# Optimization experiments

Hardware: AMD Instinct MI355X
Metric: run time of the kernel (lower is better)

The kernel has to match this reference:

```python
import jax, jax.numpy as jnp
import numpy as np
from jax import lax

VOCAB = 1000
TMAX = 1001  # max_episode_length + 1
L = 2048
H_GRU = 256


def setup_inputs() -> dict:
    key = jax.random.key(0)
    ks = jax.random.split(key, 40)
    g = lambda i, shape, s: jax.random.normal(ks[i], shape, dtype=jnp.float32) * s
    inp = {
        "x": jax.random.normal(ks[0], (1, 3, 124, 124), dtype=jnp.float32),
        "curr_instr": jax.random.randint(ks[1], (1, L), 0, VOCAB),
        "prev_instr": jax.random.randint(ks[2], (1, L), 0, VOCAB),
        "next_instr": jax.random.randint(ks[3], (1, L), 0, VOCAB),
        "tx": jax.random.randint(ks[4], (1,), 0, TMAX),
        "hx": jnp.zeros((1, 768), jnp.float32),
        "cx": jnp.zeros((1, 768), jnp.float32),
        # conv stack
        "conv1_w": g(5, (128, 3, 8, 8), 0.05), "conv1_b": jnp.zeros((128,), jnp.float32),
        "conv2_w": g(6, (64, 128, 4, 4), 0.03), "conv2_b": jnp.zeros((64,), jnp.float32),
        "conv3_w": g(7, (64, 64, 4, 4), 0.03), "conv3_b": jnp.zeros((64,), jnp.float32),
        # embeddings
        "emb": g(8, (VOCAB, 32), 0.1),
        "time_emb": g(9, (TMAX, 32), 0.1),
        # GRU (torch nn.GRU layout: 3*H rows for r,z,n)
        "gru_w_ih": g(10, (3 * H_GRU, 32), 0.1), "gru_w_hh": g(11, (3 * H_GRU, H_GRU), 0.06),
        "gru_b_ih": jnp.zeros((3 * H_GRU,), jnp.float32), "gru_b_hh": jnp.zeros((3 * H_GRU,), jnp.float32),
        # attention linear 256 -> 64
        "attn_w": g(12, (64, H_GRU), 0.06), "attn_b": jnp.zeros((64,), jnp.float32),
        # image-fusion linear 64*6*6 -> 256
        "lin_w": g(13, (256, 64 * 6 * 6), 0.02), "lin_b": jnp.zeros((256,), jnp.float32),
        # LSTMCell 768 -> 768 (torch layout: 4*H rows for i,f,g,o)
        "lstm_w_ih": g(14, (4 * 768, 768), 0.03), "lstm_w_hh": g(15, (4 * 768, 768), 0.03),
        "lstm_b_ih": jnp.zeros((4 * 768,), jnp.float32), "lstm_b_hh": jnp.zeros((4 * 768,), jnp.float32),
        # heads over [hx, time_emb] = 768 + 32 = 800
        "critic_w": g(16, (1, 800), 0.03), "critic_b": jnp.zeros((1,), jnp.float32),
        "actor_w": g(17, (4, 800), 0.01), "actor_b": jnp.zeros((4,), jnp.float32),
    }
    return inp


def _conv(x, w, b, s):
    return lax.conv_general_dilated(x, w, (s, s), "VALID") + b[None, :, None, None]


def reference(x, curr_instr, prev_instr, next_instr, tx, hx, cx,
              conv1_w, conv1_b, conv2_w, conv2_b, conv3_w, conv3_b,
              emb, time_emb, gru_w_ih, gru_w_hh, gru_b_ih, gru_b_hh,
              attn_w, attn_b, lin_w, lin_b,
              lstm_w_ih, lstm_w_hh, lstm_b_ih, lstm_b_hh,
              critic_w, critic_b, actor_w, actor_b):
    # image tower: [1,3,124,124] -> [1,64,6,6]
    h1 = jax.nn.relu(_conv(x, conv1_w, conv1_b, 4))
    h2 = jax.nn.relu(_conv(h1, conv2_w, conv2_b, 2))
    x_image_rep = jax.nn.relu(_conv(h2, conv3_w, conv3_b, 2))

    # three instruction sequences, encoded by a shared GRU (vmapped scan)
    tokens = jnp.stack([curr_instr[0], prev_instr[0], next_instr[0]])  # [3, L]

    def gru_encode(tok):
        xs = emb[tok]                               # [L, 32]
        gi_all = xs @ gru_w_ih.T + gru_b_ih         # precompute input gates [L, 3H]
        def step(h, gi):
            gh = h @ gru_w_hh.T + gru_b_hh
            i_r, i_z, i_n = jnp.split(gi, 3)
            h_r, h_z, h_n = jnp.split(gh, 3)
            r = jax.nn.sigmoid(i_r + h_r)
            z = jax.nn.sigmoid(i_z + h_z)
            n = jnp.tanh(i_n + r * h_n)
            return (1.0 - z) * n + z * h, None
        h, _ = lax.scan(step, jnp.zeros((H_GRU,), xs.dtype), gi_all)
        return h

    h3 = jax.vmap(gru_encode)(tokens)               # [3, 256]
    attn = jax.nn.sigmoid(h3 @ attn_w.T + attn_b)   # [3, 64]

    # BUG-FAITHFUL: original forward uses cached_computation['curr_x_attention']
    # for all three branches, so the three fused features are identical.
    curr_attn = attn[0][None, :, None, None]        # [1,64,1,1]
    fused = (x_image_rep * curr_attn).reshape(1, -1)  # [1, 2304]
    feat = jax.nn.relu(fused @ lin_w.T + lin_b)     # [1, 256]
    xcat = jnp.concatenate([feat, feat, feat], axis=1)  # [1, 768]

    # LSTMCell
    gates = xcat @ lstm_w_ih.T + lstm_b_ih + hx @ lstm_w_hh.T + lstm_b_hh  # [1, 3072]
    gi, gf, gg, go = jnp.split(gates, 4, axis=1)
    cx_new = jax.nn.sigmoid(gf) * cx + jax.nn.sigmoid(gi) * jnp.tanh(gg)
    hx_new = jax.nn.sigmoid(go) * jnp.tanh(cx_new)

    t = time_emb[tx].reshape(-1, 32)                # [1, 32]
    z = jnp.concatenate([hx_new, t], axis=1)        # [1, 800]
    critic = z @ critic_w.T + critic_b              # [1, 1]
    actor = z @ actor_w.T + actor_b                 # [1, 4]
    return critic, actor, hx_new, cx_new
```

## Files before the change

kernel.cpp:

```cpp
#include <hip/hip_runtime.h>
#include <hip/hip_bf16.h>
#include <stdint.h>


typedef _Float16 half8 __attribute__((ext_vector_type(8)));
typedef _Float16 half2v __attribute__((ext_vector_type(2)));
typedef float f32x4 __attribute__((ext_vector_type(4)));

__device__ __forceinline__ float sigm(float x) { return 1.0f / (1.0f + __expf(-x)); }
__device__ __forceinline__ float tanh_f(float x) { return 2.0f / (1.0f + __expf(-2.0f * x)) - 1.0f; }

__global__ void k_pack(const float* __restrict__ whh, uint32_t* __restrict__ wf16p) {
    int i = blockIdx.x * 256 + threadIdx.x;
    if (i >= 98304) return;
    half2v p = {(_Float16)whh[2 * i], (_Float16)whh[2 * i + 1]};
    wf16p[i] = __builtin_bit_cast(uint32_t, p);
}

__global__ void k_conv1(const float* __restrict__ x, const float* __restrict__ w,
                        const float* __restrict__ b, float* __restrict__ h1) {
    int idx = blockIdx.x * 256 + threadIdx.x;
    if (idx >= 128 * 30 * 30) return;
    int ox = idx % 30, oy = (idx / 30) % 30, oc = idx / 900;
    const float* wr = w + oc * 192;
    float acc = b[oc];
    for (int c = 0; c < 3; ++c)
        for (int ky = 0; ky < 8; ++ky) {
            const float* xr = x + (c * 124 + oy * 4 + ky) * 124 + ox * 4;
            const float* wk = wr + (c * 8 + ky) * 8;
#pragma unroll
            for (int kx = 0; kx < 8; ++kx) acc = fmaf(xr[kx], wk[kx], acc);
        }
    h1[idx] = fmaxf(acc, 0.0f);
}

__global__ void k_conv2(const float* __restrict__ h1, const float* __restrict__ w,
                        const float* __restrict__ b, float* __restrict__ h2) {
    int idx = blockIdx.x * 256 + threadIdx.x;
    if (idx >= 64 * 14 * 14) return;
    int ox = idx % 14, oy = (idx / 14) % 14, oc = idx / 196;
    float acc = b[oc];
    const float* wr = w + oc * 128 * 16;
    for (int c = 0; c < 128; ++c) {
#pragma unroll
        for (int ky = 0; ky < 4; ++ky) {
            const float* hr = h1 + (c * 30 + oy * 2 + ky) * 30 + ox * 2;
            const float* wk = wr + (c * 4 + ky) * 4;
#pragma unroll
            for (int kx = 0; kx < 4; ++kx) acc = fmaf(hr[kx], wk[kx], acc);
        }
    }
    h2[idx] = fmaxf(acc, 0.0f);
}

__global__ void k_conv3(const float* __restrict__ h2, const float* __restrict__ w,
                        const float* __restrict__ b, float* __restrict__ x3) {
    int idx = blockIdx.x * 256 + threadIdx.x;
    if (idx >= 64 * 6 * 6) return;
    int ox = idx % 6, oy = (idx / 6) % 6, oc = idx / 36;
    float acc = b[oc];
    const float* wr = w + oc * 64 * 16;
    for (int c = 0; c < 64; ++c) {
#pragma unroll
        for (int ky = 0; ky < 4; ++ky) {
            const float* hr = h2 + (c * 14 + oy * 2 + ky) * 14 + ox * 2;
            const float* wk = wr + (c * 4 + ky) * 4;
#pragma unroll
            for (int kx = 0; kx < 4; ++kx) acc = fmaf(hr[kx], wk[kx], acc);
        }
    }
    x3[idx] = fmaxf(acc, 0.0f);
}

__global__ void k_gi(const int* __restrict__ curr, const float* __restrict__ emb,
                     const float* __restrict__ wih, const float* __restrict__ bih,
                     float* __restrict__ gi) {
    int idx = blockIdx.x * 256 + threadIdx.x;
    int j = idx % 768, t = idx / 768;
    int tok = curr[t];
    const float4* e = (const float4*)(emb + tok * 32);
    const float4* wr = (const float4*)(wih + j * 32);
    float acc = bih[j];
#pragma unroll
    for (int k = 0; k < 8; ++k) {
        float4 ev = e[k], wv = wr[k];
        acc = fmaf(ev.x, wv.x, acc);
        acc = fmaf(ev.y, wv.y, acc);
        acc = fmaf(ev.z, wv.z, acc);
        acc = fmaf(ev.w, wv.w, acc);
    }
    gi[idx] = acc;
}

#define FOR8(X, nt) X(nt, 0) X(nt, 1) X(nt, 2) X(nt, 3) X(nt, 4) X(nt, 5) X(nt, 6) X(nt, 7)
#define FOR6(Y) Y(0) Y(1) Y(2) Y(3) Y(4) Y(5)

#define DECLB(nt, kt) uint4 b##nt##_##kt;
#define DECLBROW(nt) FOR8(DECLB, nt)
#define LOADB(nt, kt) b##nt##_##kt = wp4[nt * 512 + kt * 4 + quad];
#define LOADBROW(nt) FOR8(LOADB, nt)
#define TIEB(nt, kt) \
    asm volatile("" : "+v"(b##nt##_##kt.x), "+v"(b##nt##_##kt.y), "+v"(b##nt##_##kt.z), "+v"(b##nt##_##kt.w));
#define TIEBROW(nt) FOR8(TIEB, nt)
#define DECLBIAS(nt) const float bias##nt = bhh[wbase + nt * 16 + n16];
#define DECLACC(nt) f32x4 acc##nt;
#define ZEROACC(nt) acc##nt = (f32x4)(0.0f);
#define MF(nt, kt) \
    acc##nt = __builtin_amdgcn_mfma_f32_16x16x32_f16(a##kt, __builtin_bit_cast(half8, b##nt##_##kt), acc##nt, 0, 0, 0);
#define MFK(kt) MF(0, kt) MF(1, kt) MF(2, kt) MF(3, kt) MF(4, kt) MF(5, kt)
#define LOADA(kt) half8 a##kt = __builtin_bit_cast(half8, abase[kt * 4 + quad]);
#define EPI(nt) \
    if (lane < 16) gh[wbase + nt * 16 + lane] = acc##nt.x + acc##nt.y * 0.0009765625f + bias##nt;

__global__ __attribute__((amdgpu_flat_work_group_size(512, 512), amdgpu_waves_per_eu(2, 2)))
void k_gru_scan(const float* __restrict__ gi, const uint32_t* __restrict__ wf16p,
                const float* __restrict__ bhh, const float* __restrict__ attn_w,
                const float* __restrict__ attn_b, float* __restrict__ attn0) {
    __shared__ __align__(16) _Float16 hhi[256];
    __shared__ __align__(16) _Float16 hlo[256];
    __shared__ float gh[768];
    const int tid = threadIdx.x;
    const int lane = tid & 63;
    const int wv = tid >> 6;
    const int n16 = lane & 15;
    const int quad = lane >> 4;
    const int wbase = wv * 96;

    FOR6(DECLBROW)
    {
        const uint4* wp4 = (const uint4*)(wf16p + (size_t)(wbase + n16) * 128);
        FOR6(LOADBROW)
    }
    FOR6(TIEBROW)
    FOR6(DECLBIAS)
    FOR6(DECLACC)

    float h_own = 0.0f;
    if (tid < 256) {
        hhi[tid] = (_Float16)0.0f;
        hlo[tid] = (_Float16)0.0f;
    }
    float gv0 = 0.f, gv1 = 0.f, gv2 = 0.f;
    if (tid < 256) {
        gv0 = gi[tid];
        gv1 = gi[256 + tid];
        gv2 = gi[512 + tid];
    }
    __syncthreads();

    const uint4* abase = (n16 == 1) ? (const uint4*)hlo : (const uint4*)hhi;

#pragma clang loop unroll(disable)
    for (int step = 0; step < 2048; ++step) {
        float gn0 = 0.f, gn1 = 0.f, gn2 = 0.f;
        if (step < 2047 && tid < 256) {
            const float* gp = gi + (size_t)(step + 1) * 768 + tid;
            gn0 = gp[0]; gn1 = gp[256]; gn2 = gp[512];
        }

        FOR6(ZEROACC)
        LOADA(0) LOADA(1)
        MFK(0)
        LOADA(2)
        MFK(1)
        LOADA(3)
        MFK(2)
        LOADA(4)
        MFK(3)
        LOADA(5)
        MFK(4)
        LOADA(6)
        MFK(5)
        LOADA(7)
        MFK(6)
        MFK(7)

        FOR6(EPI)
        __syncthreads();

        if (tid < 256) {
            float r = sigm(gv0 + gh[tid]);
            float z = sigm(gv1 + gh[256 + tid]);
            float n = tanh_f(fmaf(r, gh[512 + tid], gv2));
            h_own = fmaf(z, h_own - n, n);
            _Float16 hi16 = (_Float16)h_own;
            hhi[tid] = hi16;
            hlo[tid] = (_Float16)((h_own - (float)hi16) * 1024.0f);
        }
        gv0 = gn0; gv1 = gn1; gv2 = gn2;
        __syncthreads();
    }

    if (tid < 64) {
        const float* ar = attn_w + tid * 256;
        float acc = attn_b[tid];
        for (int k = 0; k < 256; ++k) {
            float hk = (float)hhi[k] + (float)hlo[k] * 0.0009765625f;
            acc = fmaf(ar[k], hk, acc);
        }
        attn0[tid] = sigm(acc);
    }
}

__global__ void k_feat(const float* __restrict__ x3, const float* __restrict__ attn0,
                       const float* __restrict__ lw, const float* __restrict__ lb,
                       float* __restrict__ feat) {
    __shared__ __align__(16) float fused[2304];
    int t = threadIdx.x;
    for (int i = t; i < 2304; i += 64) fused[i] = x3[i] * attn0[i / 36];
    __syncthreads();
    int row = blockIdx.x * 64 + t;
    const float4* wvv = (const float4*)(lw + (size_t)row * 2304);
    float acc = lb[row];
    for (int i = 0; i < 576; ++i) {
        float4 v = wvv[i];
        const float* f = fused + i * 4;
        acc = fmaf(v.x, f[0], acc);
        acc = fmaf(v.y, f[1], acc);
        acc = fmaf(v.z, f[2], acc);
        acc = fmaf(v.w, f[3], acc);
    }
    feat[row] = fmaxf(acc, 0.0f);
}

__global__ void k_lstm_gates(const float* __restrict__ wih, const float* __restrict__ whh,
                             const float* __restrict__ bih, const float* __restrict__ bhh,
                             const float* __restrict__ hx, const float* __restrict__ feat,
                             float* __restrict__ gates) {
    int wid = threadIdx.x >> 6, lane = threadIdx.x & 63;
    int row = blockIdx.x * 4 + wid;
    const float* wi = wih + (size_t)row * 768;
    const float* wh = whh + (size_t)row * 768;
    float acc = 0.0f;
#pragma unroll
    for (int i = 0; i < 12; ++i) {
        int k = lane + i * 64;
        acc = fmaf(wi[k], feat[k & 255], acc);
        acc = fmaf(wh[k], hx[k], acc);
    }
#pragma unroll
    for (int s = 32; s; s >>= 1) acc += __shfl_down(acc, s, 64);
    if (lane == 0) gates[row] = acc + bih[row] + bhh[row];
}

__global__ void k_lstm_cell(const float* __restrict__ gates, const float* __restrict__ cx,
                            float* __restrict__ out, float* __restrict__ hxf) {
    int i = threadIdx.x;
    float g_i = gates[i], g_f = gates[768 + i], g_g = gates[1536 + i], g_o = gates[2304 + i];
    float c = cx[i];
    float cn = sigm(g_f) * c + sigm(g_i) * tanh_f(g_g);
    float hn = sigm(g_o) * tanh_f(cn);
    out[5 + i] = hn;
    out[5 + 768 + i] = cn;
    hxf[i] = hn;
}

__global__ void k_heads(const float* __restrict__ hxf, const float* __restrict__ temb,
                        const int* __restrict__ tx, const float* __restrict__ cw,
                        const float* __restrict__ cb, const float* __restrict__ aw,
                        const float* __restrict__ ab, float* __restrict__ out) {
    __shared__ float z[800];
    int t = threadIdx.x;
    for (int i = t; i < 768; i += 320) z[i] = hxf[i];
    if (t < 32) z[768 + t] = temb[tx[0] * 32 + t];
    __syncthreads();
    int w = t >> 6, lane = t & 63;
    const float* row = (w == 0) ? cw : (aw + (size_t)(w - 1) * 800);
    float acc = 0.0f;
    for (int k = lane; k < 800; k += 64) acc = fmaf(row[k], z[k], acc);
#pragma unroll
    for (int s = 32; s; s >>= 1) acc += __shfl_down(acc, s, 64);
    if (lane == 0) {
        float b = (w == 0) ? cb[0] : ab[w - 1];
        out[w] = acc + b;
    }
}

extern "C" void kernel_launch(void* const* d_in, const int* in_sizes, int n_in,
                              void* d_out, int out_size, void* d_ws, size_t ws_size,
                              hipStream_t stream) {
    const float* x = (const float*)d_in[0];
    const int* curr = (const int*)d_in[1];
    const int* tx = (const int*)d_in[4];
    const float* hx = (const float*)d_in[5];
    const float* cx = (const float*)d_in[6];
    const float* c1w = (const float*)d_in[7];
    const float* c1b = (const float*)d_in[8];
    const float* c2w = (const float*)d_in[9];
    const float* c2b = (const float*)d_in[10];
    const float* c3w = (const float*)d_in[11];
    const float* c3b = (const float*)d_in[12];
    const float* emb = (const float*)d_in[13];
    const float* temb = (const float*)d_in[14];
    const float* gwih = (const float*)d_in[15];
    const float* gwhh = (const float*)d_in[16];
    const float* gbih = (const float*)d_in[17];
    const float* gbhh = (const float*)d_in[18];
    const float* attw = (const float*)d_in[19];
    const float* attb = (const float*)d_in[20];
    const float* linw = (const float*)d_in[21];
    const float* linb = (const float*)d_in[22];
    const float* lwih = (const float*)d_in[23];
    const float* lwhh = (const float*)d_in[24];
    const float* lbih = (const float*)d_in[25];
    const float* lbhh = (const float*)d_in[26];
    const float* cw = (const float*)d_in[27];
    const float* cb = (const float*)d_in[28];
    const float* aw = (const float*)d_in[29];
    const float* ab = (const float*)d_in[30];
    float* out = (float*)d_out;

    char* ws = (char*)d_ws;
    float* gi = (float*)(ws + 0);
    float* h1 = (float*)(ws + 6291456);
    float* h2 = (float*)(ws + 6752256);
    float* x3 = (float*)(ws + 6802432);
    float* attn0 = (float*)(ws + 6811648);
    float* feat = (float*)(ws + 6811904);
    float* gates = (float*)(ws + 6812928);
    float* hxf = (float*)(ws + 6825216);
    uint32_t* wf16p = (uint32_t*)(ws + 6828288);

    k_pack<<<384, 256, 0, stream>>>(gwhh, wf16p);
    k_gi<<<6144, 256, 0, stream>>>(curr, emb, gwih, gbih, gi);
    k_conv1<<<450, 256, 0, stream>>>(x, c1w, c1b, h1);
    k_conv2<<<49, 256, 0, stream>>>(h1, c2w, c2b, h2);
    k_conv3<<<9, 256, 0, stream>>>(h2, c3w, c3b, x3);
    k_gru_scan<<<1, 512, 0, stream>>>(gi, wf16p, gbhh, attw, attb, attn0);
    k_feat<<<4, 64, 0, stream>>>(x3, attn0, linw, linb, feat);
    k_lstm_gates<<<768, 256, 0, stream>>>(lwih, lwhh, lbih, lbhh, hx, feat, gates);
    k_lstm_cell<<<1, 768, 0, stream>>>(gates, cx, out, hxf);
    k_heads<<<1, 320, 0, stream>>>(hxf, temb, tx, cw, cb, aw, ab, out);
}
```

Measured before the change: 2.569 ms.

## Remap GRU scan so each wave owns r/z/n rows, one barrier per step

Each wave now loads the W_hh rows for the r, z and n gates of the same 32 hidden units, so the gate nonlinearity and the state update run directly from MFMA accumulators in registers. This removes the shared gh staging buffer and one of the two barriers per timestep. The hidden state is double-buffered in LDS to avoid read/write races. The r and z hidden biases are folded into the precomputed input projection. The 2048-step loop is manually unrolled by two to swap the ping-pong buffers.

```diff
diff --git a/kernel.cpp b/kernel.cpp
--- a/kernel.cpp
+++ b/kernel.cpp
@@ -74,13 +74,13 @@
 
 __global__ void k_gi(const int* __restrict__ curr, const float* __restrict__ emb,
                      const float* __restrict__ wih, const float* __restrict__ bih,
-                     float* __restrict__ gi) {
+                     const float* __restrict__ bhh, float* __restrict__ gi) {
     int idx = blockIdx.x * 256 + threadIdx.x;
     int j = idx % 768, t = idx / 768;
     int tok = curr[t];
     const float4* e = (const float4*)(emb + tok * 32);
     const float4* wr = (const float4*)(wih + j * 32);
-    float acc = bih[j];
+    float acc = bih[j] + (j < 512 ? bhh[j] : 0.0f);
 #pragma unroll
     for (int k = 0; k < 8; ++k) {
         float4 ev = e[k], wv = wr[k];
@@ -97,105 +97,117 @@
 
 #define DECLB(nt, kt) uint4 b##nt##_##kt;
 #define DECLBROW(nt) FOR8(DECLB, nt)
-#define LOADB(nt, kt) b##nt##_##kt = wp4[nt * 512 + kt * 4 + quad];
-#define LOADBROW(nt) FOR8(LOADB, nt)
+#define LOADB(nt, kt) b##nt##_##kt = wp##nt[kt * 4 + quad];
+#define LOADBROW(nt) \
+    { const uint4* wp##nt = wb4 + (size_t)(TB##nt + n16) * 32; FOR8(LOADB, nt) }
 #define TIEB(nt, kt) \
     asm volatile("" : "+v"(b##nt##_##kt.x), "+v"(b##nt##_##kt.y), "+v"(b##nt##_##kt.z), "+v"(b##nt##_##kt.w));
 #define TIEBROW(nt) FOR8(TIEB, nt)
-#define DECLBIAS(nt) const float bias##nt = bhh[wbase + nt * 16 + n16];
 #define DECLACC(nt) f32x4 acc##nt;
 #define ZEROACC(nt) acc##nt = (f32x4)(0.0f);
 #define MF(nt, kt) \
     acc##nt = __builtin_amdgcn_mfma_f32_16x16x32_f16(a##kt, __builtin_bit_cast(half8, b##nt##_##kt), acc##nt, 0, 0, 0);
-#define MFK(kt) MF(0, kt) MF(1, kt) MF(2, kt) MF(3, kt) MF(4, kt) MF(5, kt)
+#define MFK(kt) MF(0, kt) MF(2, kt) MF(4, kt) MF(1, kt) MF(3, kt) MF(5, kt)
 #define LOADA(kt) half8 a##kt = __builtin_bit_cast(half8, abase[kt * 4 + quad]);
-#define EPI(nt) \
-    if (lane < 16) gh[wbase + nt * 16 + lane] = acc##nt.x + acc##nt.y * 0.0009765625f + bias##nt;
+
+#define SC 0.0009765625f
+
+#define GRU_BODY(PIN, POUT)                                                       \
+    {                                                                             \
+        float gvR0 = 0.f, gvZ0 = 0.f, gvN0 = 0.f;                                 \
+        float gvR1 = 0.f, gvZ1 = 0.f, gvN1 = 0.f;                                 \
+        if (lane < 16) {                                                          \
+            gvR0 = gp[0];  gvZ0 = gp[256]; gvN0 = gp[512];                        \
+            gvR1 = gp[16]; gvZ1 = gp[272]; gvN1 = gp[528];                        \
+        }                                                                         \
+        gp += 768;                                                                \
+        const uint4* abase = (n16 == 1) ? (const uint4*)hbuf[PIN][1]              \
+                                        : (const uint4*)hbuf[PIN][0];             \
+        FOR6(ZEROACC)                                                             \
+        LOADA(0) LOADA(1)                                                         \
+        MFK(0)                                                                    \
+        LOADA(2)                                                                  \
+        MFK(1)                                                                    \
+        LOADA(3)                                                                  \
+        MFK(2)                                                                    \
+        LOADA(4)                                                                  \
+        MFK(3)                                                                    \
+        LOADA(5)                                                                  \
+        MFK(4)                                                                    \
+        LOADA(6)                                                                  \
+        MFK(5)                                                                    \
+        LOADA(7)                                                                  \
+        MFK(6)                                                                    \
+        MFK(7)                                                                    \
+        if (lane < 16) {                                                          \
+            float yR0 = fmaf(acc0.y, SC, acc0.x) + gvR0;                          \
+            float yZ0 = fmaf(acc2.y, SC, acc2.x) + gvZ0;                          \
+            float yN0 = fmaf(acc4.y, SC, acc4.x) + bN0;                           \
+            float r0 = sigm(yR0), z0 = sigm(yZ0);                                 \
+            float n0 = tanh_f(fmaf(r0, yN0, gvN0));                               \
+            h0 = fmaf(z0, h0 - n0, n0);                                           \
+            float yR1 = fmaf(acc1.y, SC, acc1.x) + gvR1;                          \
+            float yZ1 = fmaf(acc3.y, SC, acc3.x) + gvZ1;                          \
+            float yN1 = fmaf(acc5.y, SC, acc5.x) + bN1;                           \
+            float r1 = sigm(yR1), z1 = sigm(yZ1);                                 \
+            float n1 = tanh_f(fmaf(r1, yN1, gvN1));                               \
+            h1 = fmaf(z1, h1 - n1, n1);                                           \
+            _Float16 hi0 = (_Float16)h0, hi1 = (_Float16)h1;                      \
+            hbuf[POUT][0][e0] = hi0;                                              \
+            hbuf[POUT][1][e0] = (_Float16)((h0 - (float)hi0) * 1024.0f);          \
+            hbuf[POUT][0][e1] = hi1;                                              \
+            hbuf[POUT][1][e1] = (_Float16)((h1 - (float)hi1) * 1024.0f);          \
+        }                                                                         \
+        __syncthreads();                                                          \
+    }
 
 __global__ __attribute__((amdgpu_flat_work_group_size(512, 512), amdgpu_waves_per_eu(2, 2)))
 void k_gru_scan(const float* __restrict__ gi, const uint32_t* __restrict__ wf16p,
                 const float* __restrict__ bhh, const float* __restrict__ attn_w,
                 const float* __restrict__ attn_b, float* __restrict__ attn0) {
-    __shared__ __align__(16) _Float16 hhi[256];
-    __shared__ __align__(16) _Float16 hlo[256];
-    __shared__ float gh[768];
+    __shared__ __align__(16) _Float16 hbuf[2][2][256];
     const int tid = threadIdx.x;
     const int lane = tid & 63;
     const int wv = tid >> 6;
     const int n16 = lane & 15;
     const int quad = lane >> 4;
-    const int wbase = wv * 96;
+
+    const int TB0 = 32 * wv, TB1 = TB0 + 16;
+    const int TB2 = 256 + TB0, TB3 = 256 + TB1;
+    const int TB4 = 512 + TB0, TB5 = 512 + TB1;
+    const int e0 = TB0 + n16, e1 = TB1 + n16;
 
     FOR6(DECLBROW)
     {
-        const uint4* wp4 = (const uint4*)(wf16p + (size_t)(wbase + n16) * 128);
+        const uint4* wb4 = (const uint4*)wf16p;
         FOR6(LOADBROW)
     }
     FOR6(TIEBROW)
-    FOR6(DECLBIAS)
     FOR6(DECLACC)
 
-    float h_own = 0.0f;
+    const float bN0 = bhh[512 + e0];
+    const float bN1 = bhh[512 + e1];
+
+    float h0 = 0.0f, h1 = 0.0f;
     if (tid < 256) {
-        hhi[tid] = (_Float16)0.0f;
-        hlo[tid] = (_Float16)0.0f;
-    }
-    float gv0 = 0.f, gv1 = 0.f, gv2 = 0.f;
-    if (tid < 256) {
-        gv0 = gi[tid];
-        gv1 = gi[256 + tid];
-        gv2 = gi[512 + tid];
+        hbuf[0][0][tid] = (_Float16)0.0f;
+        hbuf[0][1][tid] = (_Float16)0.0f;
     }
     __syncthreads();
 
-    const uint4* abase = (n16 == 1) ? (const uint4*)hlo : (const uint4*)hhi;
+    const float* gp = gi + e0;
 
 #pragma clang loop unroll(disable)
-    for (int step = 0; step < 2048; ++step) {
-        float gn0 = 0.f, gn1 = 0.f, gn2 = 0.f;
-        if (step < 2047 && tid < 256) {
-            const float* gp = gi + (size_t)(step + 1) * 768 + tid;
-            gn0 = gp[0]; gn1 = gp[256]; gn2 = gp[512];
-        }
-
-        FOR6(ZEROACC)
-        LOADA(0) LOADA(1)
-        MFK(0)
-        LOADA(2)
-        MFK(1)
-        LOADA(3)
-        MFK(2)
-        LOADA(4)
-        MFK(3)
-        LOADA(5)
-        MFK(4)
-        LOADA(6)
-        MFK(5)
-        LOADA(7)
-        MFK(6)
-        MFK(7)
-
-        FOR6(EPI)
-        __syncthreads();
-
-        if (tid < 256) {
-            float r = sigm(gv0 + gh[tid]);
-            float z = sigm(gv1 + gh[256 + tid]);
-            float n = tanh_f(fmaf(r, gh[512 + tid], gv2));
-            h_own = fmaf(z, h_own - n, n);
-            _Float16 hi16 = (_Float16)h_own;
-            hhi[tid] = hi16;
-            hlo[tid] = (_Float16)((h_own - (float)hi16) * 1024.0f);
-        }
-        gv0 = gn0; gv1 = gn1; gv2 = gn2;
-        __syncthreads();
+    for (int it = 0; it < 1024; ++it) {
+        GRU_BODY(0, 1)
+        GRU_BODY(1, 0)
     }
 
     if (tid < 64) {
         const float* ar = attn_w + tid * 256;
         float acc = attn_b[tid];
         for (int k = 0; k < 256; ++k) {
-            float hk = (float)hhi[k] + (float)hlo[k] * 0.0009765625f;
+            float hk = (float)hbuf[0][0][k] + (float)hbuf[0][1][k] * SC;
             acc = fmaf(ar[k], hk, acc);
         }
         attn0[tid] = sigm(acc);
@@ -322,7 +334,7 @@
     uint32_t* wf16p = (uint32_t*)(ws + 6828288);
 
     k_pack<<<384, 256, 0, stream>>>(gwhh, wf16p);
-    k_gi<<<6144, 256, 0, stream>>>(curr, emb, gwih, gbih, gi);
+    k_gi<<<6144, 256, 0, stream>>>(curr, emb, gwih, gbih, gbhh, gi);
     k_conv1<<<450, 256, 0, stream>>>(x, c1w, c1b, h1);
     k_conv2<<<49, 256, 0, stream>>>(h1, c2w, c2b, h2);
     k_conv3<<<9, 256, 0, stream>>>(h2, c3w, c3b, x3);
```

Result: slower. 2.625 ms (+2.2%).
